# Kernel optimization log

Measured on AMD Instinct MI355X. Metric: run time of the kernel, lower is better.

## Reference

```python
import jax, jax.numpy as jnp
import numpy as np

B, V, H = 16384, 1024, 256


def setup_inputs() -> dict:
    key = jax.random.key(0)
    k1, k2 = jax.random.split(key)
    # binary spin configurations in {0,1}
    batch = jax.random.bernoulli(k1, 0.5, (B, V)).astype(jnp.float32)
    # small weights + negative hidden bias keep exp(log p*) finite in fp32
    weights_amp = jax.random.normal(k2, (H, V), dtype=jnp.float32) * (0.05 / np.sqrt(V))
    visible_bias_amp = jnp.zeros((V,), dtype=jnp.float32)
    hidden_bias_amp = -5.0 * jnp.ones((H,), dtype=jnp.float32)
    return {
        'batch': batch,
        'weights_amp': weights_amp,
        'visible_bias_amp': visible_bias_amp,
        'hidden_bias_amp': hidden_bias_amp,
        'k': 8,
    }


def _gibbs_sampling_amp(v0, W, vb, hb, k, key):
    """k steps of block Gibbs sampling, vectorized over the whole batch [B,V]."""
    keys = jax.random.split(key, 2 * k).reshape(k, 2)

    def step(v, ks):
        ph = jax.nn.sigmoid(v @ W.T + hb)                      # [B,H]
        h = (jax.random.uniform(ks[0], ph.shape) < ph).astype(v.dtype)
        pv = jax.nn.sigmoid(h @ W + vb)                        # [B,V]
        v = (jax.random.uniform(ks[1], pv.shape) < pv).astype(v.dtype)
        return v, None

    vk, _ = jax.lax.scan(step, v0, keys)
    return vk


def reference(batch, weights_amp, visible_bias_amp, hidden_bias_amp, k):
    W, vb, hb = weights_amp, visible_bias_amp, hidden_bias_amp
    nbatch = batch.shape[0]
    key = jax.random.key(42)

    vk = _gibbs_sampling_amp(batch, W, vb, hb, k, key)          # [B,V]

    ph0 = jax.nn.sigmoid(batch @ W.T + hb)                      # [B,H] positive-phase hidden probs
    pre_k = vk @ W.T + hb                                       # [B,H]
    phk = jax.nn.sigmoid(pre_k)                                 # [B,H] negative-phase hidden probs

    # unnormalized_probability_amp(vk) = exp(vk.vb + sum_j softplus((W vk + hb)_j))
    log_p = vk @ vb + jax.nn.softplus(pre_k).sum(axis=-1)       # [B]
    inv_norm = jnp.exp(-log_p) / nbatch                         # 1 / (len(batch) * p*(vk))

    # g_W = sum_b [outer(phk_b, vk_b) - outer(ph0_b, v0_b)] / norm_b
    g_w = (jnp.einsum('b,bh,bv->hv', inv_norm, phk, vk)
           - jnp.einsum('b,bh,bv->hv', inv_norm, ph0, batch))   # [H,V]
    g_vb = jnp.einsum('b,bv->v', inv_norm, vk - batch)          # [V]
    g_hb = jnp.einsum('b,bh->h', inv_norm, phk - ph0)           # [H]

    return jnp.concatenate([g_w.ravel(), g_vb, g_hb])
```

## Files before the change

kernel.cpp:

```cpp
#include <hip/hip_runtime.h>
#include <stdint.h>

#define B_DIM 16384
#define V_DIM 1024
#define H_DIM 256
#define K_STEPS 8
#define HALF_B 8192

typedef short bf16x8 __attribute__((ext_vector_type(8)));
typedef float f32x4 __attribute__((ext_vector_type(4)));

__host__ __device__ inline uint32_t rotl32(uint32_t v, int r) {
#if defined(__HIP_DEVICE_COMPILE__)
    return __builtin_amdgcn_alignbit(v, v, (uint32_t)(32 - r));
#else
    return (v << r) | (v >> (32 - r));
#endif
}

__host__ __device__ inline void threefry2x32(uint32_t k0, uint32_t k1,
                                             uint32_t x0, uint32_t x1,
                                             uint32_t* o0, uint32_t* o1) {
    uint32_t k2 = k0 ^ k1 ^ 0x1BD11BDAu;
    x0 += k0; x1 += k1;
#define TF_RND(r) { x0 += x1; x1 = rotl32(x1, (r)); x1 ^= x0; }
    TF_RND(13) TF_RND(15) TF_RND(26) TF_RND(6)
    x0 += k1; x1 += k2 + 1u;
    TF_RND(17) TF_RND(29) TF_RND(16) TF_RND(24)
    x0 += k2; x1 += k0 + 2u;
    TF_RND(13) TF_RND(15) TF_RND(26) TF_RND(6)
    x0 += k0; x1 += k1 + 3u;
    TF_RND(17) TF_RND(29) TF_RND(16) TF_RND(24)
    x0 += k1; x1 += k2 + 4u;
    TF_RND(13) TF_RND(15) TF_RND(26) TF_RND(6)
    x0 += k2; x1 += k0 + 5u;
#undef TF_RND
    *o0 = x0; *o1 = x1;
}

__device__ inline float tf_uniform(uint32_t key0, uint32_t key1, uint32_t e) {
    uint32_t o0, o1;
    threefry2x32(key0, key1, 0u, e, &o0, &o1);
    uint32_t bits = o0 ^ o1;
    return __uint_as_float((bits >> 9) | 0x3f800000u) - 1.0f;
}

__device__ inline uint16_t bf16_rn(float f) {
    uint32_t u = __float_as_uint(f);
    uint32_t r = u + 0x7FFFu + ((u >> 16) & 1u);
    return (uint16_t)(r >> 16);
}
__device__ inline float bf16_to_f32(uint16_t h) {
    return __uint_as_float(((uint32_t)h) << 16);
}

__device__ inline void gload_lds16(const void* g, void* l) {
    __builtin_amdgcn_global_load_lds((const __attribute__((address_space(1))) uint32_t*)g,
                                     (__attribute__((address_space(3))) uint32_t*)l, 16, 0, 0);
}

template <int MODE>
__device__ __forceinline__ void gemm_block(
    const int m0, const int n0,
    const ushort* __restrict__ A, const ushort* __restrict__ Bhi,
    const ushort* __restrict__ Blo, const float* __restrict__ bias,
    ushort* __restrict__ out, ushort* __restrict__ out2,
    const int N, const int K, const uint32_t key0, const uint32_t key1,
    ushort* Am, ushort* Bm) {
    const int tid = threadIdx.x;
    const int lane = tid & 63;
    const int w = tid >> 6;
    const int wm = (w & 1) * 32;
    const int wn = (w >> 1) * 32;
    const int q = lane >> 4;
    const int l15 = lane & 15;

    const ushort* asrc[2];
#pragma unroll
    for (int i = 0; i < 2; ++i) {
        const int j = w * 2 + i;
        const int row = j * 8 + (lane >> 3);
        const int sl = (lane & 7) ^ (row & 7);
        asrc[i] = A + (size_t)(m0 + row) * K + (sl >> 2) * 32 + (sl & 3) * 8;
    }
    const ushort* bsrc[4];
#pragma unroll
    for (int i = 0; i < 4; ++i) {
        const int j = w * 4 + i;
        const int row = j * 4 + (lane >> 4);
        const int sl = (lane & 15) ^ (row & 15);
        const int hl = (sl >> 2) & 1;
        bsrc[i] = (hl ? Blo : Bhi) + (size_t)(n0 + row) * K + (sl >> 3) * 32 + (sl & 3) * 8;
    }

    f32x4 acc[2][2] = {};

    for (int k0 = 0; k0 < K; k0 += 64) {
#pragma unroll
        for (int i = 0; i < 2; ++i)
            gload_lds16(asrc[i] + k0, &Am[(w * 2 + i) * 512]);
#pragma unroll
        for (int i = 0; i < 4; ++i)
            gload_lds16(bsrc[i] + k0, &Bm[(w * 4 + i) * 512]);
        __syncthreads();
#pragma unroll
        for (int s = 0; s < 2; ++s) {
            bf16x8 af[2], bh[2], bl[2];
#pragma unroll
            for (int i = 0; i < 2; ++i) {
                const int ra = wm + i * 16 + l15;
                af[i] = *(const bf16x8*)((const char*)Am + ra * 128 +
                                         (((s * 4 + q) ^ (ra & 7)) * 16));
            }
#pragma unroll
            for (int j = 0; j < 2; ++j) {
                const int rb = wn + j * 16 + l15;
                const char* bb = (const char*)Bm + rb * 256;
                bh[j] = *(const bf16x8*)(bb + (((s * 8 + q) ^ (rb & 15)) * 16));
                bl[j] = *(const bf16x8*)(bb + (((s * 8 + 4 + q) ^ (rb & 15)) * 16));
            }
#pragma unroll
            for (int i = 0; i < 2; ++i)
#pragma unroll
                for (int j = 0; j < 2; ++j) {
                    acc[i][j] = __builtin_amdgcn_mfma_f32_16x16x32_bf16(af[i], bh[j], acc[i][j], 0, 0, 0);
                    acc[i][j] = __builtin_amdgcn_mfma_f32_16x16x32_bf16(af[i], bl[j], acc[i][j], 0, 0, 0);
                }
        }
        __syncthreads();
    }

    const int orow = q * 4;
#pragma unroll
    for (int i = 0; i < 2; ++i) {
#pragma unroll
        for (int j = 0; j < 2; ++j) {
            int col = n0 + wn + j * 16 + l15;
            float bv = bias[col];
#pragma unroll
            for (int r = 0; r < 4; ++r) {
                int row = m0 + wm + i * 16 + orow + r;
                float val = acc[i][j][r] + bv;
                if (MODE == 0) {
                    float E = expf(-val);
                    uint32_t e = (uint32_t)row * (uint32_t)N + (uint32_t)col;
                    float u = tf_uniform(key0, key1, e);
                    out[(size_t)row * N + col] = (fmaf(u, E, u) < 1.0f) ? (ushort)0x3F80 : (ushort)0;
                } else if (MODE == 3) {
                    float E = expf(-val);
                    float sg = 1.0f / (1.0f + E);
                    uint32_t e = (uint32_t)row * (uint32_t)N + (uint32_t)col;
                    float u = tf_uniform(key0, key1, e);
                    out[(size_t)row * N + col] = (fmaf(u, E, u) < 1.0f) ? (ushort)0x3F80 : (ushort)0;
                    out2[(size_t)row * N + col] = bf16_rn(sg);
                } else {
                    float sg = 1.0f / (1.0f + expf(-val));
                    out[(size_t)row * N + col] = bf16_rn(sg);
                }
            }
        }
    }
}

__device__ __forceinline__ void vsample_block(
    const ushort* __restrict__ h, const float* __restrict__ W,
    const float* __restrict__ vb, ushort* __restrict__ vout,
    uint32_t key0, uint32_t key1, int row_base) {
    const int lane = threadIdx.x & 63;
    const int wid = threadIdx.x >> 6;

    float vbr[16];
#pragma unroll
    for (int t = 0; t < 16; ++t) vbr[t] = vb[lane + 64 * t];

    const int rb2 = row_base + wid * 2;
#pragma unroll
    for (int rr = 0; rr < 2; ++rr) {
        const int b = rb2 + rr;
        ushort4 hv = ((const ushort4*)(h + (size_t)b * H_DIM))[lane];
        unsigned long long masks[4];
        masks[0] = __ballot(hv.x != 0);
        masks[1] = __ballot(hv.y != 0);
        masks[2] = __ballot(hv.z != 0);
        masks[3] = __ballot(hv.w != 0);

        float acc[16];
#pragma unroll
        for (int t = 0; t < 16; ++t) acc[t] = 0.0f;

#pragma unroll
        for (int s = 0; s < 4; ++s) {
            unsigned long long m = masks[s];
            while (m) {
                int l = __ffsll(m) - 1;
                m &= m - 1;
                int j = l * 4 + s;
                const float* wrow = W + (size_t)j * V_DIM + lane;
#pragma unroll
                for (int t = 0; t < 16; ++t) acc[t] += wrow[64 * t];
            }
        }

        const uint32_t ebase = (uint32_t)b * (uint32_t)V_DIM + (uint32_t)lane;
        ushort* orow = vout + (size_t)b * V_DIM + lane;
#pragma unroll
        for (int t = 0; t < 16; ++t) {
            float pre = acc[t] + vbr[t];
            float E = expf(-pre);
            float u = tf_uniform(key0, key1, ebase + 64u * (uint32_t)t);
            orow[64 * t] = (fmaf(u, E, u) < 1.0f) ? (ushort)0x3F80 : (ushort)0;
        }
    }
}

template <int MODE>
__global__ __launch_bounds__(256, 4) void gemm_only(
    const ushort* __restrict__ A, const ushort* __restrict__ Bhi,
    const ushort* __restrict__ Blo, const float* __restrict__ bias,
    ushort* __restrict__ out, ushort* __restrict__ out2,
    uint32_t key0, uint32_t key1, int mbase) {
    __shared__ __align__(16) ushort Am[64 * 64];
    __shared__ __align__(16) ushort Bm[64 * 128];
    gemm_block<MODE>(mbase + blockIdx.x * 64, blockIdx.y * 64, A, Bhi, Blo, bias,
                     out, out2, H_DIM, V_DIM, key0, key1, Am, Bm);
}

template <int MODE>
__global__ __launch_bounds__(256, 4) void hybrid_step(
    const ushort* __restrict__ vin, const ushort* __restrict__ Whi,
    const ushort* __restrict__ Wlo, const float* __restrict__ hb,
    ushort* __restrict__ hout, ushort* __restrict__ out2,
    uint32_t gk0, uint32_t gk1, int gemm_mbase,
    const ushort* __restrict__ hprev, const float* __restrict__ Wf,
    const float* __restrict__ vb, ushort* __restrict__ vout,
    uint32_t vk0, uint32_t vk1, int vs_base, int nb_vs) {
    __shared__ __align__(16) ushort Am[64 * 64];
    __shared__ __align__(16) ushort Bm[64 * 128];
    const int bid = blockIdx.x;
    if (bid < nb_vs) {
        vsample_block(hprev, Wf, vb, vout, vk0, vk1, vs_base + bid * 8);
    } else {
        const int g = bid - nb_vs;
        const int gx = g & 127;
        const int gy = g >> 7;
        gemm_block<MODE>(gemm_mbase + gx * 64, gy * 64, vin, Whi, Wlo, hb,
                         hout, out2, H_DIM, V_DIM, gk0, gk1, Am, Bm);
    }
}

__global__ __launch_bounds__(256, 4) void mfma_gemm_acc(
    const ushort* __restrict__ A, const ushort* __restrict__ Bt,
    float* __restrict__ out, int N, int K, int k_slice) {
    __shared__ __align__(16) ushort As[64 * 64];
    __shared__ __align__(16) ushort Bs[64 * 64];

    const int tid = threadIdx.x;
    const int lane = tid & 63;
    const int w = tid >> 6;
    const int m0 = blockIdx.x * 64;
    const int n0 = blockIdx.y * 64;
    const int kbase = blockIdx.z * k_slice;

    const int wm = (w & 1) * 32;
    const int wn = (w >> 1) * 32;
    const int q = lane >> 4;
    const int l15 = lane & 15;

    const ushort* asrc[2];
    const ushort* bsrc[2];
#pragma unroll
    for (int i = 0; i < 2; ++i) {
        const int j = w * 2 + i;
        const int row = j * 8 + (lane >> 3);
        const int sl = (lane & 7) ^ (row & 7);
        const size_t off = (size_t)row * K + (sl >> 2) * 32 + (sl & 3) * 8;
        asrc[i] = A + (size_t)m0 * K + off;
        bsrc[i] = Bt + (size_t)n0 * K + off;
    }

    f32x4 acc[2][2] = {};

    for (int kt = 0; kt < k_slice; kt += 64) {
        const int k0 = kbase + kt;
#pragma unroll
        for (int i = 0; i < 2; ++i) {
            gload_lds16(asrc[i] + k0, &As[(w * 2 + i) * 512]);
            gload_lds16(bsrc[i] + k0, &Bs[(w * 2 + i) * 512]);
        }
        __syncthreads();
#pragma unroll
        for (int s = 0; s < 2; ++s) {
            bf16x8 af[2], bf[2];
#pragma unroll
            for (int i = 0; i < 2; ++i) {
                const int ra = wm + i * 16 + l15;
                const int rb = wn + i * 16 + l15;
                af[i] = *(const bf16x8*)((const char*)As + ra * 128 +
                                         (((s * 4 + q) ^ (ra & 7)) * 16));
                bf[i] = *(const bf16x8*)((const char*)Bs + rb * 128 +
                                         (((s * 4 + q) ^ (rb & 7)) * 16));
            }
#pragma unroll
            for (int i = 0; i < 2; ++i)
#pragma unroll
                for (int j = 0; j < 2; ++j)
                    acc[i][j] = __builtin_amdgcn_mfma_f32_16x16x32_bf16(af[i], bf[j], acc[i][j], 0, 0, 0);
        }
        __syncthreads();
    }

    const int orow = q * 4;
#pragma unroll
    for (int i = 0; i < 2; ++i)
#pragma unroll
        for (int j = 0; j < 2; ++j) {
            int col = n0 + wn + j * 16 + l15;
#pragma unroll
            for (int r = 0; r < 4; ++r) {
                int row = m0 + wm + i * 16 + orow + r;
                atomicAdd(&out[(size_t)row * N + col], acc[i][j][r]);
            }
        }
}

__global__ void wsplit_kernel(const float* __restrict__ W, ushort* __restrict__ whi,
                              ushort* __restrict__ wlo) {
    int idx = blockIdx.x * 256 + threadIdx.x;
    float w = W[idx];
    ushort hi = bf16_rn(w);
    float fhi = bf16_to_f32(hi);
    ushort lo = bf16_rn(w - fhi);
    whi[idx] = hi; wlo[idx] = lo;
}

__global__ void tobf16_kernel(const float* __restrict__ src, ushort* __restrict__ dst) {
    int idx = blockIdx.x * 256 + threadIdx.x;
    float4 f = ((const float4*)src)[idx];
    ushort4 o;
    o.x = bf16_rn(f.x); o.y = bf16_rn(f.y); o.z = bf16_rn(f.z); o.w = bf16_rn(f.w);
    ((ushort4*)dst)[idx] = o;
}

__global__ __launch_bounds__(256) void lognorm_kernel(
    const ushort* __restrict__ phk, const ushort* __restrict__ vk,
    const float* __restrict__ vb, float* __restrict__ inv) {
    int b = blockIdx.x;
    int tid = threadIdx.x;
    float p = bf16_to_f32(phk[(size_t)b * H_DIM + tid]);
    float s = -log1pf(-p);
    for (int j = tid; j < V_DIM; j += 256)
        s += bf16_to_f32(vk[(size_t)b * V_DIM + j]) * vb[j];
    for (int off = 32; off > 0; off >>= 1) s += __shfl_down(s, off, 64);
    __shared__ float wsum[4];
    int lane = tid & 63, wid = tid >> 6;
    if (lane == 0) wsum[wid] = s;
    __syncthreads();
    if (tid == 0) {
        float t = wsum[0] + wsum[1] + wsum[2] + wsum[3];
        inv[b] = expf(-t) * (1.0f / 16384.0f);
    }
}

__global__ void build_At(const ushort* __restrict__ P, const float* __restrict__ inv,
                         float sgn, ushort* __restrict__ At) {
    __shared__ float T[64][65];
    int c = threadIdx.x & 63;
    int rb = threadIdx.x >> 6;
    int b0 = blockIdx.x * 64;
    int h0 = blockIdx.y * 64;
    for (int r = rb; r < 64; r += 4) {
        int b = b0 + r;
        T[c][r] = sgn * inv[b] * bf16_to_f32(P[(size_t)b * H_DIM + h0 + c]);
    }
    __syncthreads();
    for (int r = rb; r < 64; r += 4)
        At[(size_t)(h0 + r) * B_DIM + b0 + c] = bf16_rn(T[r][c]);
}

__global__ void build_Bt(const ushort* __restrict__ Sb, const float* __restrict__ Sf,
                         int use_f32, ushort* __restrict__ Bt) {
    __shared__ ushort T[64][65];
    int c = threadIdx.x & 63;
    int rb = threadIdx.x >> 6;
    int b0 = blockIdx.x * 64;
    int v0 = blockIdx.y * 64;
    for (int r = rb; r < 64; r += 4) {
        int b = b0 + r;
        T[c][r] = use_f32 ? bf16_rn(Sf[(size_t)b * V_DIM + v0 + c])
                          : Sb[(size_t)b * V_DIM + v0 + c];
    }
    __syncthreads();
    for (int r = rb; r < 64; r += 4)
        Bt[(size_t)(v0 + r) * B_DIM + b0 + c] = T[r][c];
}

__global__ void gvb_kernel(const ushort* __restrict__ vk, const ushort* __restrict__ vbat,
                           const float* __restrict__ inv, float* __restrict__ gvb) {
    int col = blockIdx.x * 256 + threadIdx.x;
    int b0 = blockIdx.y * 512;
    float acc = 0.0f;
    for (int r = 0; r < 512; ++r) {
        int b = b0 + r;
        acc += inv[b] * (bf16_to_f32(vk[(size_t)b * V_DIM + col]) -
                         bf16_to_f32(vbat[(size_t)b * V_DIM + col]));
    }
    atomicAdd(&gvb[col], acc);
}

__global__ void ghb_kernel(const ushort* __restrict__ phk, const ushort* __restrict__ ph0,
                           const float* __restrict__ inv, float* __restrict__ ghb) {
    int col = threadIdx.x;
    int b0 = blockIdx.x * 256;
    float acc = 0.0f;
    for (int r = 0; r < 256; ++r) {
        int b = b0 + r;
        acc += inv[b] * (bf16_to_f32(phk[(size_t)b * H_DIM + col]) -
                         bf16_to_f32(ph0[(size_t)b * H_DIM + col]));
    }
    atomicAdd(&ghb[col], acc);
}

extern "C" void kernel_launch(void* const* d_in, const int* in_sizes, int n_in,
                              void* d_out, int out_size, void* d_ws, size_t ws_size,
                              hipStream_t stream) {
    const float* batch = (const float*)d_in[0];
    const float* W = (const float*)d_in[1];
    const float* vb = (const float*)d_in[2];
    const float* hb = (const float*)d_in[3];

    char* base = (char*)d_ws;
    ushort* w_hi  = (ushort*)(base + 0);
    ushort* w_lo  = (ushort*)(base + 524288);
    ushort* v_cur = (ushort*)(base + 2097152);
    float*  inv   = (float*)(base + 35651584);
    ushort* h_cur = (ushort*)(base + 35717120);
    ushort* At    = h_cur;
    ushort* batch_bf = (ushort*)(base + 44105728);
    ushort* Bt    = batch_bf;
    ushort* ph0b  = (ushort*)(base + 77660160);
    ushort* phkb  = (ushort*)(base + 86048768);

    float* gw  = (float*)d_out;
    float* gvb = gw + (size_t)H_DIM * V_DIM;
    float* ghb = gvb + V_DIM;

    hipMemsetAsync(d_out, 0, (size_t)out_size * sizeof(float), stream);

    uint32_t sk0[16], sk1[16];
    for (int n = 0; n < 16; ++n) threefry2x32(0u, 42u, 0u, (uint32_t)n, &sk0[n], &sk1[n]);

    wsplit_kernel<<<dim3(1024), dim3(256), 0, stream>>>(W, w_hi, w_lo);
    tobf16_kernel<<<dim3(B_DIM * V_DIM / 4 / 256), dim3(256), 0, stream>>>(batch, batch_bf);

    const int NB_VS = HALF_B / 8;
    const int NB_G  = (HALF_B / 64) * 4;
    const dim3 HYB(NB_VS + NB_G);

    gemm_only<3><<<dim3(128, 4), dim3(256), 0, stream>>>(
        batch_bf, w_hi, w_lo, hb, h_cur, ph0b, sk0[0], sk1[0], 0);

    for (int s = 0; s < K_STEPS; ++s) {
        const ushort* vin = (s == 0) ? batch_bf : v_cur;
        if (s == 0) {
            hybrid_step<3><<<HYB, dim3(256), 0, stream>>>(
                vin, w_hi, w_lo, hb, h_cur, ph0b, sk0[0], sk1[0], HALF_B,
                h_cur, W, vb, v_cur, sk0[1], sk1[1], 0, NB_VS);
        } else {
            hybrid_step<0><<<HYB, dim3(256), 0, stream>>>(
                vin, w_hi, w_lo, hb, h_cur, nullptr, sk0[2 * s], sk1[2 * s], HALF_B,
                h_cur, W, vb, v_cur, sk0[2 * s + 1], sk1[2 * s + 1], 0, NB_VS);
        }
        if (s < K_STEPS - 1) {
            hybrid_step<0><<<HYB, dim3(256), 0, stream>>>(
                v_cur, w_hi, w_lo, hb, h_cur, nullptr, sk0[2 * s + 2], sk1[2 * s + 2], 0,
                h_cur, W, vb, v_cur, sk0[2 * s + 1], sk1[2 * s + 1], HALF_B, NB_VS);
        } else {
            hybrid_step<1><<<HYB, dim3(256), 0, stream>>>(
                v_cur, w_hi, w_lo, hb, phkb, nullptr, 0u, 0u, 0,
                h_cur, W, vb, v_cur, sk0[2 * s + 1], sk1[2 * s + 1], HALF_B, NB_VS);
        }
    }
    gemm_only<1><<<dim3(128, 4), dim3(256), 0, stream>>>(
        v_cur, w_hi, w_lo, hb, phkb, nullptr, 0u, 0u, HALF_B);

    lognorm_kernel<<<dim3(B_DIM), dim3(256), 0, stream>>>(phkb, v_cur, vb, inv);
    ghb_kernel<<<dim3(B_DIM / 256), dim3(256), 0, stream>>>(phkb, ph0b, inv, ghb);
    gvb_kernel<<<dim3(V_DIM / 256, B_DIM / 512), dim3(256), 0, stream>>>(v_cur, batch_bf, inv, gvb);

    build_At<<<dim3(B_DIM / 64, H_DIM / 64), dim3(256), 0, stream>>>(phkb, inv, 1.0f, At);
    build_Bt<<<dim3(B_DIM / 64, V_DIM / 64), dim3(256), 0, stream>>>(v_cur, nullptr, 0, Bt);
    mfma_gemm_acc<<<dim3(H_DIM / 64, V_DIM / 64, 16), dim3(256), 0, stream>>>(
        At, Bt, gw, V_DIM, B_DIM, 1024);
    build_At<<<dim3(B_DIM / 64, H_DIM / 64), dim3(256), 0, stream>>>(ph0b, inv, -1.0f, At);
    build_Bt<<<dim3(B_DIM / 64, V_DIM / 64), dim3(256), 0, stream>>>(nullptr, batch, 1, Bt);
    mfma_gemm_acc<<<dim3(H_DIM / 64, V_DIM / 64, 16), dim3(256), 0, stream>>>(
        At, Bt, gw, V_DIM, B_DIM, 1024);
}
```

Before: 859.2 us.

## Pre-pack GEMM operands into MFMA fragment order and drop LDS staging

Weights, the input batch and the sampled visible state are now written in a layout where each MFMA lane's bf16x8 fragment sits contiguous in global memory. The hidden-probability GEMM then loads fragments straight from global/L2 with no shared memory and no barriers, and occupancy hint rises to 6 blocks per CU. The visible sampler writes the packed layout every step and the row-major copy only on the final step. This removes LDS traffic and syncs, but global loads are no longer cooperatively shared across waves, so A/B tiles are re-read per wave from cache.

Result: slower. 887.2 us (+3.3%).

```diff
diff --git a/kernel.cpp b/kernel.cpp
--- a/kernel.cpp
+++ b/kernel.cpp
@@ -59,65 +59,70 @@
                                      (__attribute__((address_space(3))) uint32_t*)l, 16, 0, 0);
 }
 
+
+__global__ void pack_w_kernel(const float* __restrict__ W,
+                              ushort* __restrict__ whp, ushort* __restrict__ wlp) {
+    int uid = blockIdx.x * 256 + threadIdx.x;
+    int l = uid & 63, s = (uid >> 6) & 1, kc = (uid >> 7) & 15, R = uid >> 11;
+    int row = R * 16 + (l & 15);
+    int col = kc * 64 + s * 32 + (l >> 4) * 8;
+    const float* src = W + (size_t)row * V_DIM + col;
+    ushort* dh = whp + (size_t)uid * 8;
+    ushort* dl = wlp + (size_t)uid * 8;
+#pragma unroll
+    for (int e = 0; e < 8; ++e) {
+        float w = src[e];
+        ushort hi = bf16_rn(w);
+        dh[e] = hi;
+        dl[e] = bf16_rn(w - bf16_to_f32(hi));
+    }
+}
+
+__global__ void pack_batch_kernel(const float* __restrict__ batch,
+                                  ushort* __restrict__ bp) {
+    int uid = blockIdx.x * 256 + threadIdx.x;
+    int l = uid & 63, s = (uid >> 6) & 1, kc = (uid >> 7) & 15, R = uid >> 11;
+    int row = R * 16 + (l & 15);
+    int col = kc * 64 + s * 32 + (l >> 4) * 8;
+    const float* src = batch + (size_t)row * V_DIM + col;
+    ushort* d = bp + (size_t)uid * 8;
+#pragma unroll
+    for (int e = 0; e < 8; ++e) d[e] = bf16_rn(src[e]);
+}
+
 template <int MODE>
-__device__ __forceinline__ void gemm_block(
+__device__ __forceinline__ void gemm_block_p(
     const int m0, const int n0,
-    const ushort* __restrict__ A, const ushort* __restrict__ Bhi,
-    const ushort* __restrict__ Blo, const float* __restrict__ bias,
+    const ushort* __restrict__ Ap, const ushort* __restrict__ Bhp,
+    const ushort* __restrict__ Blp, const float* __restrict__ bias,
     ushort* __restrict__ out, ushort* __restrict__ out2,
-    const int N, const int K, const uint32_t key0, const uint32_t key1,
-    ushort* Am, ushort* Bm) {
-    const int tid = threadIdx.x;
-    const int lane = tid & 63;
-    const int w = tid >> 6;
+    const uint32_t key0, const uint32_t key1) {
+    const int lane = threadIdx.x & 63;
+    const int w = threadIdx.x >> 6;
     const int wm = (w & 1) * 32;
     const int wn = (w >> 1) * 32;
     const int q = lane >> 4;
     const int l15 = lane & 15;
 
-    const ushort* asrc[2];
-#pragma unroll
-    for (int i = 0; i < 2; ++i) {
-        const int j = w * 2 + i;
-        const int row = j * 8 + (lane >> 3);
-        const int sl = (lane & 7) ^ (row & 7);
-        asrc[i] = A + (size_t)(m0 + row) * K + (sl >> 2) * 32 + (sl & 3) * 8;
-    }
-    const ushort* bsrc[4];
-#pragma unroll
-    for (int i = 0; i < 4; ++i) {
-        const int j = w * 4 + i;
-        const int row = j * 4 + (lane >> 4);
-        const int sl = (lane & 15) ^ (row & 15);
-        const int hl = (sl >> 2) & 1;
-        bsrc[i] = (hl ? Blo : Bhi) + (size_t)(n0 + row) * K + (sl >> 3) * 32 + (sl & 3) * 8;
-    }
+    const ushort* apA = Ap + (size_t)((m0 >> 4) + (wm >> 4)) * 16384 + lane * 8;
+    const ushort* apBh = Bhp + (size_t)((n0 >> 4) + (wn >> 4)) * 16384 + lane * 8;
+    const ushort* apBl = Blp + (size_t)((n0 >> 4) + (wn >> 4)) * 16384 + lane * 8;
 
     f32x4 acc[2][2] = {};
 
-    for (int k0 = 0; k0 < K; k0 += 64) {
-#pragma unroll
-        for (int i = 0; i < 2; ++i)
-            gload_lds16(asrc[i] + k0, &Am[(w * 2 + i) * 512]);
-#pragma unroll
-        for (int i = 0; i < 4; ++i)
-            gload_lds16(bsrc[i] + k0, &Bm[(w * 4 + i) * 512]);
-        __syncthreads();
+#pragma unroll 2
+    for (int kc = 0; kc < 16; ++kc) {
 #pragma unroll
         for (int s = 0; s < 2; ++s) {
+            const int go = kc * 1024 + s * 512;
             bf16x8 af[2], bh[2], bl[2];
 #pragma unroll
-            for (int i = 0; i < 2; ++i) {
-                const int ra = wm + i * 16 + l15;
-                af[i] = *(const bf16x8*)((const char*)Am + ra * 128 +
-                                         (((s * 4 + q) ^ (ra & 7)) * 16));
-            }
+            for (int i = 0; i < 2; ++i)
+                af[i] = *(const bf16x8*)(apA + go + i * 16384);
 #pragma unroll
             for (int j = 0; j < 2; ++j) {
-                const int rb = wn + j * 16 + l15;
-                const char* bb = (const char*)Bm + rb * 256;
-                bh[j] = *(const bf16x8*)(bb + (((s * 8 + q) ^ (rb & 15)) * 16));
-                bl[j] = *(const bf16x8*)(bb + (((s * 8 + 4 + q) ^ (rb & 15)) * 16));
+                bh[j] = *(const bf16x8*)(apBh + go + j * 16384);
+                bl[j] = *(const bf16x8*)(apBl + go + j * 16384);
             }
 #pragma unroll
             for (int i = 0; i < 2; ++i)
@@ -127,7 +132,6 @@
                     acc[i][j] = __builtin_amdgcn_mfma_f32_16x16x32_bf16(af[i], bl[j], acc[i][j], 0, 0, 0);
                 }
         }
-        __syncthreads();
     }
 
     const int orow = q * 4;
@@ -143,19 +147,19 @@
                 float val = acc[i][j][r] + bv;
                 if (MODE == 0) {
                     float E = expf(-val);
-                    uint32_t e = (uint32_t)row * (uint32_t)N + (uint32_t)col;
+                    uint32_t e = (uint32_t)row * (uint32_t)H_DIM + (uint32_t)col;
                     float u = tf_uniform(key0, key1, e);
-                    out[(size_t)row * N + col] = (fmaf(u, E, u) < 1.0f) ? (ushort)0x3F80 : (ushort)0;
+                    out[(size_t)row * H_DIM + col] = (fmaf(u, E, u) < 1.0f) ? (ushort)0x3F80 : (ushort)0;
                 } else if (MODE == 3) {
                     float E = expf(-val);
                     float sg = 1.0f / (1.0f + E);
-                    uint32_t e = (uint32_t)row * (uint32_t)N + (uint32_t)col;
+                    uint32_t e = (uint32_t)row * (uint32_t)H_DIM + (uint32_t)col;
                     float u = tf_uniform(key0, key1, e);
-                    out[(size_t)row * N + col] = (fmaf(u, E, u) < 1.0f) ? (ushort)0x3F80 : (ushort)0;
-                    out2[(size_t)row * N + col] = bf16_rn(sg);
+                    out[(size_t)row * H_DIM + col] = (fmaf(u, E, u) < 1.0f) ? (ushort)0x3F80 : (ushort)0;
+                    out2[(size_t)row * H_DIM + col] = bf16_rn(sg);
                 } else {
                     float sg = 1.0f / (1.0f + expf(-val));
-                    out[(size_t)row * N + col] = bf16_rn(sg);
+                    out[(size_t)row * H_DIM + col] = bf16_rn(sg);
                 }
             }
         }
@@ -164,7 +168,8 @@
 
 __device__ __forceinline__ void vsample_block(
     const ushort* __restrict__ h, const float* __restrict__ W,
-    const float* __restrict__ vb, ushort* __restrict__ vout,
+    const float* __restrict__ vb, ushort* __restrict__ vpack,
+    ushort* __restrict__ vrow, int write_row,
     uint32_t key0, uint32_t key1, int row_base) {
     const int lane = threadIdx.x & 63;
     const int wid = threadIdx.x >> 6;
@@ -202,49 +207,51 @@
         }
 
         const uint32_t ebase = (uint32_t)b * (uint32_t)V_DIM + (uint32_t)lane;
-        ushort* orow = vout + (size_t)b * V_DIM + lane;
+        ushort* vp = vpack + (size_t)(b >> 4) * 16384 + (b & 15) * 8 +
+                     ((lane >> 5) & 1) * 512 + ((lane >> 3) & 3) * 128 + (lane & 7);
+        ushort* orow = vrow + (size_t)b * V_DIM + lane;
 #pragma unroll
         for (int t = 0; t < 16; ++t) {
             float pre = acc[t] + vbr[t];
             float E = expf(-pre);
             float u = tf_uniform(key0, key1, ebase + 64u * (uint32_t)t);
-            orow[64 * t] = (fmaf(u, E, u) < 1.0f) ? (ushort)0x3F80 : (ushort)0;
+            ushort val = (fmaf(u, E, u) < 1.0f) ? (ushort)0x3F80 : (ushort)0;
+            vp[t * 1024] = val;
+            if (write_row) orow[64 * t] = val;
         }
     }
 }
 
 template <int MODE>
-__global__ __launch_bounds__(256, 4) void gemm_only(
-    const ushort* __restrict__ A, const ushort* __restrict__ Bhi,
-    const ushort* __restrict__ Blo, const float* __restrict__ bias,
+__global__ __launch_bounds__(256, 6) void gemm_only(
+    const ushort* __restrict__ Ap, const ushort* __restrict__ Bhp,
+    const ushort* __restrict__ Blp, const float* __restrict__ bias,
     ushort* __restrict__ out, ushort* __restrict__ out2,
     uint32_t key0, uint32_t key1, int mbase) {
-    __shared__ __align__(16) ushort Am[64 * 64];
-    __shared__ __align__(16) ushort Bm[64 * 128];
-    gemm_block<MODE>(mbase + blockIdx.x * 64, blockIdx.y * 64, A, Bhi, Blo, bias,
-                     out, out2, H_DIM, V_DIM, key0, key1, Am, Bm);
+    gemm_block_p<MODE>(mbase + blockIdx.x * 64, blockIdx.y * 64, Ap, Bhp, Blp,
+                       bias, out, out2, key0, key1);
 }
 
 template <int MODE>
-__global__ __launch_bounds__(256, 4) void hybrid_step(
-    const ushort* __restrict__ vin, const ushort* __restrict__ Whi,
-    const ushort* __restrict__ Wlo, const float* __restrict__ hb,
+__global__ __launch_bounds__(256, 6) void hybrid_step(
+    const ushort* __restrict__ Ap, const ushort* __restrict__ Whp,
+    const ushort* __restrict__ Wlp, const float* __restrict__ hb,
     ushort* __restrict__ hout, ushort* __restrict__ out2,
     uint32_t gk0, uint32_t gk1, int gemm_mbase,
     const ushort* __restrict__ hprev, const float* __restrict__ Wf,
-    const float* __restrict__ vb, ushort* __restrict__ vout,
+    const float* __restrict__ vb, ushort* __restrict__ vpack,
+    ushort* __restrict__ vrow, int write_row,
     uint32_t vk0, uint32_t vk1, int vs_base, int nb_vs) {
-    __shared__ __align__(16) ushort Am[64 * 64];
-    __shared__ __align__(16) ushort Bm[64 * 128];
     const int bid = blockIdx.x;
     if (bid < nb_vs) {
-        vsample_block(hprev, Wf, vb, vout, vk0, vk1, vs_base + bid * 8);
+        vsample_block(hprev, Wf, vb, vpack, vrow, write_row, vk0, vk1,
+                      vs_base + bid * 8);
     } else {
         const int g = bid - nb_vs;
         const int gx = g & 127;
         const int gy = g >> 7;
-        gemm_block<MODE>(gemm_mbase + gx * 64, gy * 64, vin, Whi, Wlo, hb,
-                         hout, out2, H_DIM, V_DIM, gk0, gk1, Am, Bm);
+        gemm_block_p<MODE>(gemm_mbase + gx * 64, gy * 64, Ap, Whp, Wlp, hb,
+                           hout, out2, gk0, gk1);
     }
 }
 
@@ -321,24 +328,6 @@
                 atomicAdd(&out[(size_t)row * N + col], acc[i][j][r]);
             }
         }
-}
-
-__global__ void wsplit_kernel(const float* __restrict__ W, ushort* __restrict__ whi,
-                              ushort* __restrict__ wlo) {
-    int idx = blockIdx.x * 256 + threadIdx.x;
-    float w = W[idx];
-    ushort hi = bf16_rn(w);
-    float fhi = bf16_to_f32(hi);
-    ushort lo = bf16_rn(w - fhi);
-    whi[idx] = hi; wlo[idx] = lo;
-}
-
-__global__ void tobf16_kernel(const float* __restrict__ src, ushort* __restrict__ dst) {
-    int idx = blockIdx.x * 256 + threadIdx.x;
-    float4 f = ((const float4*)src)[idx];
-    ushort4 o;
-    o.x = bf16_rn(f.x); o.y = bf16_rn(f.y); o.z = bf16_rn(f.z); o.w = bf16_rn(f.w);
-    ((ushort4*)dst)[idx] = o;
 }
 
 __global__ __launch_bounds__(256) void lognorm_kernel(
@@ -394,7 +383,7 @@
         Bt[(size_t)(v0 + r) * B_DIM + b0 + c] = T[r][c];
 }
 
-__global__ void gvb_kernel(const ushort* __restrict__ vk, const ushort* __restrict__ vbat,
+__global__ void gvb_kernel(const ushort* __restrict__ vk, const float* __restrict__ batchf,
                            const float* __restrict__ inv, float* __restrict__ gvb) {
     int col = blockIdx.x * 256 + threadIdx.x;
     int b0 = blockIdx.y * 512;
@@ -402,7 +391,7 @@
     for (int r = 0; r < 512; ++r) {
         int b = b0 + r;
         acc += inv[b] * (bf16_to_f32(vk[(size_t)b * V_DIM + col]) -
-                         bf16_to_f32(vbat[(size_t)b * V_DIM + col]));
+                         batchf[(size_t)b * V_DIM + col]);
     }
     atomicAdd(&gvb[col], acc);
 }
@@ -429,16 +418,17 @@
     const float* hb = (const float*)d_in[3];
 
     char* base = (char*)d_ws;
-    ushort* w_hi  = (ushort*)(base + 0);
-    ushort* w_lo  = (ushort*)(base + 524288);
-    ushort* v_cur = (ushort*)(base + 2097152);
-    float*  inv   = (float*)(base + 35651584);
-    ushort* h_cur = (ushort*)(base + 35717120);
-    ushort* At    = h_cur;
-    ushort* batch_bf = (ushort*)(base + 44105728);
-    ushort* Bt    = batch_bf;
-    ushort* ph0b  = (ushort*)(base + 77660160);
-    ushort* phkb  = (ushort*)(base + 86048768);
+    ushort* w_hi_p = (ushort*)(base + 0);
+    ushort* w_lo_p = (ushort*)(base + 524288);
+    float*  inv    = (float*)(base + 1048576);
+    ushort* v_pack = (ushort*)(base + 2097152);
+    ushort* Bt     = v_pack;
+    ushort* v_row  = (ushort*)(base + 35651584);
+    ushort* batch_p = v_row;
+    ushort* h_cur  = (ushort*)(base + 69206016);
+    ushort* At     = h_cur;
+    ushort* ph0b   = (ushort*)(base + 77594624);
+    ushort* phkb   = (ushort*)(base + 85983232);
 
     float* gw  = (float*)d_out;
     float* gvb = gw + (size_t)H_DIM * V_DIM;
@@ -449,46 +439,46 @@
     uint32_t sk0[16], sk1[16];
     for (int n = 0; n < 16; ++n) threefry2x32(0u, 42u, 0u, (uint32_t)n, &sk0[n], &sk1[n]);
 
-    wsplit_kernel<<<dim3(1024), dim3(256), 0, stream>>>(W, w_hi, w_lo);
-    tobf16_kernel<<<dim3(B_DIM * V_DIM / 4 / 256), dim3(256), 0, stream>>>(batch, batch_bf);
+    pack_w_kernel<<<dim3(128), dim3(256), 0, stream>>>(W, w_hi_p, w_lo_p);
+    pack_batch_kernel<<<dim3(8192), dim3(256), 0, stream>>>(batch, batch_p);
 
     const int NB_VS = HALF_B / 8;
     const int NB_G  = (HALF_B / 64) * 4;
     const dim3 HYB(NB_VS + NB_G);
 
     gemm_only<3><<<dim3(128, 4), dim3(256), 0, stream>>>(
-        batch_bf, w_hi, w_lo, hb, h_cur, ph0b, sk0[0], sk1[0], 0);
+        batch_p, w_hi_p, w_lo_p, hb, h_cur, ph0b, sk0[0], sk1[0], 0);
 
     for (int s = 0; s < K_STEPS; ++s) {
-        const ushort* vin = (s == 0) ? batch_bf : v_cur;
+        const int wr = (s == K_STEPS - 1) ? 1 : 0;
         if (s == 0) {
             hybrid_step<3><<<HYB, dim3(256), 0, stream>>>(
-                vin, w_hi, w_lo, hb, h_cur, ph0b, sk0[0], sk1[0], HALF_B,
-                h_cur, W, vb, v_cur, sk0[1], sk1[1], 0, NB_VS);
+                batch_p, w_hi_p, w_lo_p, hb, h_cur, ph0b, sk0[0], sk1[0], HALF_B,
+                h_cur, W, vb, v_pack, v_row, wr, sk0[1], sk1[1], 0, NB_VS);
         } else {
             hybrid_step<0><<<HYB, dim3(256), 0, stream>>>(
-                vin, w_hi, w_lo, hb, h_cur, nullptr, sk0[2 * s], sk1[2 * s], HALF_B,
-                h_cur, W, vb, v_cur, sk0[2 * s + 1], sk1[2 * s + 1], 0, NB_VS);
+                v_pack, w_hi_p, w_lo_p, hb, h_cur, nullptr, sk0[2 * s], sk1[2 * s], HALF_B,
+                h_cur, W, vb, v_pack, v_row, wr, sk0[2 * s + 1], sk1[2 * s + 1], 0, NB_VS);
         }
         if (s < K_STEPS - 1) {
             hybrid_step<0><<<HYB, dim3(256), 0, stream>>>(
-                v_cur, w_hi, w_lo, hb, h_cur, nullptr, sk0[2 * s + 2], sk1[2 * s + 2], 0,
-                h_cur, W, vb, v_cur, sk0[2 * s + 1], sk1[2 * s + 1], HALF_B, NB_VS);
+                v_pack, w_hi_p, w_lo_p, hb, h_cur, nullptr, sk0[2 * s + 2], sk1[2 * s + 2], 0,
+                h_cur, W, vb, v_pack, v_row, wr, sk0[2 * s + 1], sk1[2 * s + 1], HALF_B, NB_VS);
         } else {
             hybrid_step<1><<<HYB, dim3(256), 0, stream>>>(
-                v_cur, w_hi, w_lo, hb, phkb, nullptr, 0u, 0u, 0,
-                h_cur, W, vb, v_cur, sk0[2 * s + 1], sk1[2 * s + 1], HALF_B, NB_VS);
+                v_pack, w_hi_p, w_lo_p, hb, phkb, nullptr, 0u, 0u, 0,
+                h_cur, W, vb, v_pack, v_row, wr, sk0[2 * s + 1], sk1[2 * s + 1], HALF_B, NB_VS);
         }
     }
     gemm_only<1><<<dim3(128, 4), dim3(256), 0, stream>>>(
-        v_cur, w_hi, w_lo, hb, phkb, nullptr, 0u, 0u, HALF_B);
-
-    lognorm_kernel<<<dim3(B_DIM), dim3(256), 0, stream>>>(phkb, v_cur, vb, inv);
+        v_pack, w_hi_p, w_lo_p, hb, phkb, nullptr, 0u, 0u, HALF_B);
+
+    lognorm_kernel<<<dim3(B_DIM), dim3(256), 0, stream>>>(phkb, v_row, vb, inv);
     ghb_kernel<<<dim3(B_DIM / 256), dim3(256), 0, stream>>>(phkb, ph0b, inv, ghb);
-    gvb_kernel<<<dim3(V_DIM / 256, B_DIM / 512), dim3(256), 0, stream>>>(v_cur, batch_bf, inv, gvb);
+    gvb_kernel<<<dim3(V_DIM / 256, B_DIM / 512), dim3(256), 0, stream>>>(v_row, batch, inv, gvb);
 
     build_At<<<dim3(B_DIM / 64, H_DIM / 64), dim3(256), 0, stream>>>(phkb, inv, 1.0f, At);
-    build_Bt<<<dim3(B_DIM / 64, V_DIM / 64), dim3(256), 0, stream>>>(v_cur, nullptr, 0, Bt);
+    build_Bt<<<dim3(B_DIM / 64, V_DIM / 64), dim3(256), 0, stream>>>(v_row, nullptr, 0, Bt);
     mfma_gemm_acc<<<dim3(H_DIM / 64, V_DIM / 64, 16), dim3(256), 0, stream>>>(
         At, Bt, gw, V_DIM, B_DIM, 1024);
     build_At<<<dim3(B_DIM / 64, H_DIM / 64), dim3(256), 0, stream>>>(ph0b, inv, -1.0f, At);
```
